# Kernel tuning notes

Hardware: AMD Instinct MI355X
Metric: run time of the kernel (lower is better)

## Reference

```python
import jax, jax.numpy as jnp
import numpy as np

T, B, Y, X, C = 9, 2, 128, 128, 64
W = (T - 1) // 2
WIN, HEADS = 8, 4
EPS = 1e-3  # keras LayerNormalization default epsilon


def _get_indices(center, size):
    right = list(range(center, size, 2))
    left = list(range(center - 2, -1, -2))
    idx = np.array(left[::-1] + right, dtype=np.int32)
    return np.clip(idx, 1, size - 2)


def _pyramid_indices(t):
    levels = []
    size, center = t, (t - 1) // 2
    while size > 1:
        c = _get_indices(center, size)
        levels.append((c - 1, c, c + 1))
        center = int(np.where(c == center)[0][0])
        size = len(c)
    return levels


LEVELS = _pyramid_indices(T)            # 3 levels for T=9: sizes 5, 3, 1
CIN = [C * (l + 1) for l in range(len(LEVELS))]    # 64, 128, 192
COUT = [C * (l + 2) for l in range(len(LEVELS))]   # 128, 192, 256


def _window_attention(q, kv, wqkv, bqkv, wo, bo):
    # WindowSpatialAttention: non-overlapping WINxWIN windows, MHA of q over kv.
    N, Yd, Xd, Cd = q.shape
    w, h = WIN, HEADS
    dh = Cd // h
    nY, nX = Yd // w, Xd // w

    def to_win(t):
        t = t.reshape(N, nY, w, nX, w, Cd).transpose(0, 1, 3, 2, 4, 5)
        return t.reshape(N * nY * nX, w * w, Cd)

    qw, kvw = to_win(q), to_win(kv)
    qp = (qw @ wqkv[0] + bqkv[0]).reshape(-1, w * w, h, dh)
    kp = (kvw @ wqkv[1] + bqkv[1]).reshape(-1, w * w, h, dh)
    vp = (kvw @ wqkv[2] + bqkv[2]).reshape(-1, w * w, h, dh)
    logits = jnp.einsum('nqhd,nkhd->nhqk', qp, kp) / jnp.sqrt(jnp.float32(dh))
    attn = jax.nn.softmax(logits, axis=-1)
    out = jnp.einsum('nhqk,nkhd->nqhd', attn, vp).reshape(-1, w * w, Cd)
    out = out @ wo + bo
    out = out.reshape(N, nY, nX, w, w, Cd).transpose(0, 1, 3, 2, 4, 5)
    return out.reshape(N, Yd, Xd, Cd)


def _forward(x, params):
    fidx = np.arange(T) - W  # relative frame indices, static (non frame-aware)
    current = x
    level1 = None
    for l, (pi, ci, ni) in enumerate(LEVELS):
        emb, lng, lnb, wqkv, bqkv, wo, bo, cw, cb = params[l]
        cin = current.shape[-1]
        # additive relative temporal embedding, indexed by frame offset + W
        t_emb = emb[fidx + W]                       # [Tl, cin]
        cur = current + t_emb[:, None, None, None, :]
        mu = cur.mean(-1, keepdims=True)
        var = cur.var(-1, keepdims=True)
        cur = (cur - mu) * jax.lax.rsqrt(var + EPS) * lng + lnb
        S = len(ci)
        prev = cur[pi].reshape(S * B, Y, X, cin)
        cen = cur[ci].reshape(S * B, Y, X, cin)
        nxt = cur[ni].reshape(S * B, Y, X, cin)
        q = jnp.concatenate([cen, prev, cen, nxt], axis=0)
        kv = jnp.concatenate([prev, cen, nxt, cen], axis=0)
        att = _window_attention(q, kv, wqkv, bqkv, wo, bo)
        parts = jnp.split(att, 4, axis=0)           # SplitBatch(n_splits=4)
        comb = jnp.concatenate(parts, axis=-1)      # Combine: concat + 1x1 conv
        down = jax.nn.relu(comb @ cw + cb)
        if S > 1:
            down = down.reshape(S, B, Y, X, down.shape[-1])
        if l == 0:
            level1 = down
        current = down
        fidx = fidx[ci]
    return current, level1


def setup_inputs() -> dict:
    key = jax.random.key(0)
    ks = iter(jax.random.split(key, 64))
    inp = {'x': jax.random.normal(next(ks), (T, B, Y, X, C), jnp.float32)}
    for l, (ci, co) in enumerate(zip(CIN, COUT)):
        inp[f'emb{l}'] = 0.02 * jax.random.normal(next(ks), (T, ci), jnp.float32)
        inp[f'lng{l}'] = jnp.ones((ci,), jnp.float32)
        inp[f'lnb{l}'] = jnp.zeros((ci,), jnp.float32)
        inp[f'wqkv{l}'] = 0.02 * jax.random.normal(next(ks), (3, ci, ci), jnp.float32)
        inp[f'bqkv{l}'] = jnp.zeros((3, ci), jnp.float32)
        inp[f'wo{l}'] = 0.02 * jax.random.normal(next(ks), (ci, ci), jnp.float32)
        inp[f'bo{l}'] = jnp.zeros((ci,), jnp.float32)
        inp[f'cw{l}'] = 0.02 * jax.random.normal(next(ks), (4 * ci, co), jnp.float32)
        inp[f'cb{l}'] = jnp.zeros((co,), jnp.float32)
    return inp


def reference(x, emb0, lng0, lnb0, wqkv0, bqkv0, wo0, bo0, cw0, cb0,
              emb1, lng1, lnb1, wqkv1, bqkv1, wo1, bo1, cw1, cb1,
              emb2, lng2, lnb2, wqkv2, bqkv2, wo2, bo2, cw2, cb2):
    params = [
        (emb0, lng0, lnb0, wqkv0, bqkv0, wo0, bo0, cw0, cb0),
        (emb1, lng1, lnb1, wqkv1, bqkv1, wo1, bo1, cw1, cb1),
        (emb2, lng2, lnb2, wqkv2, bqkv2, wo2, bo2, cw2, cb2),
    ]
    return _forward(x, params)
```

## Files before the change

kernel.cpp:

```cpp
#include <hip/hip_runtime.h>

typedef _Float16 f16;
typedef f16 f16x4 __attribute__((ext_vector_type(4)));
typedef f16 f16x8 __attribute__((ext_vector_type(8)));
typedef float f32x4 __attribute__((ext_vector_type(4)));

#define MFMA16(a, b, c) __builtin_amdgcn_mfma_f32_16x16x16f16((a), (b), (c), 0, 0, 0)
#define MFMA32(a, b, c) __builtin_amdgcn_mfma_f32_16x16x32_f16((a), (b), (c), 0, 0, 0)

struct Meta   { int pi[5], ci[5], ni[5]; };
struct EmbMap { int m[9]; };

template <int CIN>
__global__ __launch_bounds__(64) void wT_kernel(const float* __restrict__ wqkv,
                                                f16* __restrict__ wqkvT) {
  int j = blockIdx.x;
  int which = j / CIN, jj = j % CIN;
  const float* src = wqkv + (long)which * CIN * CIN + jj;
  f16* dst = wqkvT + (long)j * CIN;
  for (int c = threadIdx.x; c < CIN; c += 64) dst[c] = (f16)src[(long)c * CIN];
}

template <int CIN, int CO>
__global__ __launch_bounds__(256) void woc_kernel(
    const float* __restrict__ wo, const float* __restrict__ bo,
    const float* __restrict__ cw, const float* __restrict__ cb,
    f16* __restrict__ wocA, float* __restrict__ fb) {
  __shared__ float scw[4 * CIN];
  __shared__ float red[256];
  int o = blockIdx.x;
  for (int i = threadIdx.x; i < 4 * CIN; i += 256) scw[i] = cw[(long)i * CO + o];
  __syncthreads();
  for (int pm = threadIdx.x; pm < 4 * CIN; pm += 256) {
    int p = pm / CIN, mm = pm % CIN;
    const float* wr = wo + (long)mm * CIN;
    const float* sc = scw + p * CIN;
    float s = 0.f;
    for (int c = 0; c < CIN; ++c) s += wr[c] * sc[c];
    wocA[((long)(pm >> 3) * CO + o) * 8 + (pm & 7)] = (f16)s;
  }
  float part = 0.f;
  for (int i = threadIdx.x; i < 4 * CIN; i += 256) part += bo[i % CIN] * scw[i];
  red[threadIdx.x] = part;
  __syncthreads();
  for (int st = 128; st > 0; st >>= 1) {
    if (threadIdx.x < st) red[threadIdx.x] += red[threadIdx.x + st];
    __syncthreads();
  }
  if (threadIdx.x == 0) fb[o] = cb[o] + red[0];
}

template <typename InT, int CIN>
__global__ __launch_bounds__(256) void lnproj_kernel(
    const InT* __restrict__ in, const float* __restrict__ emb,
    const float* __restrict__ lng, const float* __restrict__ lnb,
    const f16* __restrict__ wT, const float* __restrict__ bqkv,
    f16* __restrict__ gq, f16* __restrict__ gk, f16* __restrict__ gvt,
    EmbMap em) {
  constexpr int KS = CIN / 32;
  constexpr int NT = CIN / 16;
  constexpr int C8 = CIN / 8;
  __shared__ f16 sB[CIN * CIN];
  int which = blockIdx.x;
  long win = blockIdx.y;
  long img = win >> 8;
  int wid = (int)(win & 255);
  int wy = wid >> 4, wx = wid & 15;
  int w = threadIdx.x >> 6, lane = threadIdx.x & 63;
  int r16 = lane & 15, kq = lane >> 4;
  int tok = w * 16 + r16;
  long orig = img * 16384 + (long)(wy * 8 + (tok >> 3)) * 128 + wx * 8 + (tok & 7);
  const InT* arow = in + orig * CIN + kq * 8;
  int t = (int)(img >> 1);
  const float* er = emb + (long)em.m[t] * CIN + kq * 8;

  float v[KS][8];
  float s = 0.f;
#pragma unroll
  for (int ks = 0; ks < KS; ++ks) {
    f32x4 e0 = *(const f32x4*)(er + ks * 32);
    f32x4 e1 = *(const f32x4*)(er + ks * 32 + 4);
    if constexpr (sizeof(InT) == 4) {
      f32x4 x0 = *(const f32x4*)((const float*)arow + ks * 32);
      f32x4 x1 = *(const f32x4*)((const float*)arow + ks * 32 + 4);
#pragma unroll
      for (int j = 0; j < 4; ++j) { v[ks][j] = x0[j] + e0[j]; v[ks][4 + j] = x1[j] + e1[j]; }
    } else {
      f16x8 x = *(const f16x8*)((const f16*)arow + ks * 32);
#pragma unroll
      for (int j = 0; j < 4; ++j) { v[ks][j] = (float)x[j] + e0[j]; v[ks][4 + j] = (float)x[4 + j] + e1[j]; }
    }
#pragma unroll
    for (int j = 0; j < 8; ++j) s += v[ks][j];
  }
  s += __shfl_xor(s, 16);
  s += __shfl_xor(s, 32);
  float mu = s * (1.f / CIN);
  float ssd = 0.f;
#pragma unroll
  for (int ks = 0; ks < KS; ++ks)
#pragma unroll
    for (int j = 0; j < 8; ++j) { float d = v[ks][j] - mu; ssd += d * d; }
  ssd += __shfl_xor(ssd, 16);
  ssd += __shfl_xor(ssd, 32);
  float inv = rsqrtf(ssd * (1.f / CIN) + 1e-3f);
  f16x8 a[KS];
#pragma unroll
  for (int ks = 0; ks < KS; ++ks) {
    f32x4 g0 = *(const f32x4*)(lng + ks * 32 + kq * 8);
    f32x4 g1 = *(const f32x4*)(lng + ks * 32 + kq * 8 + 4);
    f32x4 b0 = *(const f32x4*)(lnb + ks * 32 + kq * 8);
    f32x4 b1 = *(const f32x4*)(lnb + ks * 32 + kq * 8 + 4);
#pragma unroll
    for (int j = 0; j < 4; ++j) {
      a[ks][j] = (f16)((v[ks][j] - mu) * inv * g0[j] + b0[j]);
      a[ks][4 + j] = (f16)((v[ks][4 + j] - mu) * inv * g1[j] + b1[j]);
    }
  }

  const f16* wsrc = wT + (long)which * CIN * CIN;
  for (int idx = threadIdx.x; idx < CIN * C8; idx += 256) {
    int j = idx / C8, c8 = idx % C8;
    f16x8 vv = *(const f16x8*)(wsrc + idx * 8);
    int off = ((j * CIN + c8 * 8) * 2) ^ ((j & 7) << 4);
    *(f16x8*)((char*)sB + off) = vv;
  }
  __syncthreads();

  f32x4 acc[NT] = {};
#pragma unroll
  for (int ks = 0; ks < KS; ++ks) {
#pragma unroll
    for (int tt = 0; tt < NT; ++tt) {
      int off = (((tt * 16 + r16) * CIN + ks * 32 + kq * 8) * 2) ^ ((r16 & 7) << 4);
      f16x8 bb = *(const f16x8*)((char*)sB + off);
      acc[tt] = MFMA32(a[ks], bb, acc[tt]);
    }
  }
  __syncthreads();

  if (which < 2) {
#pragma unroll
    for (int tt = 0; tt < NT; ++tt) {
      float bias = bqkv[which * CIN + tt * 16 + r16];
#pragma unroll
      for (int rg = 0; rg < 4; ++rg) {
        int r = w * 16 + kq * 4 + rg;
        int c = tt * 16 + r16;
        int off = ((r * CIN + c) * 2) ^ ((r & 7) << 4);
        *(f16*)((char*)sB + off) = (f16)(acc[tt][rg] + bias);
      }
    }
    __syncthreads();
    f16* dst = (which ? gk : gq) + win * 64 * CIN;
    for (int idx = threadIdx.x; idx < 64 * C8; idx += 256) {
      int r = idx / C8, c8 = idx % C8;
      int off = ((r * CIN + c8 * 8) * 2) ^ ((r & 7) << 4);
      f16x8 vv = *(const f16x8*)((char*)sB + off);
      *(f16x8*)(dst + r * CIN + c8 * 8) = vv;
    }
  } else {
#pragma unroll
    for (int tt = 0; tt < NT; ++tt) {
      float bias = bqkv[2 * CIN + tt * 16 + r16];
#pragma unroll
      for (int rg = 0; rg < 4; ++rg) {
        int c = tt * 16 + r16;
        int pos = w * 16 + kq * 4 + rg;
        int off = ((c * 64 + pos) * 2) ^ ((c & 7) << 4);
        *(f16*)((char*)sB + off) = (f16)(acc[tt][rg] + bias);
      }
    }
    __syncthreads();
    for (int c = threadIdx.x; c < CIN; c += 256) {
      f16* dst = gvt + (win * CIN + c) * 64;
#pragma unroll
      for (int p8 = 0; p8 < 8; ++p8) {
        int off = ((c * 64 + p8 * 8) * 2) ^ ((c & 7) << 4);
        *(f16x8*)(dst + p8 * 8) = *(const f16x8*)((char*)sB + off);
      }
    }
  }
}

template <int CIN, int DH, int CO>
__global__ __launch_bounds__(256) void attn4_kernel(
    const f16* __restrict__ gq, const f16* __restrict__ gk,
    const f16* __restrict__ gvt, const f16* __restrict__ wocA,
    const float* __restrict__ fb, float* __restrict__ out, Meta m) {
  constexpr int NKS = DH / 16;
  constexpr int NK8 = DH / 32;
  constexpr int NK4 = (DH % 32) / 16;
  constexpr int CO4 = CO / 4;
  constexpr int NTC = CO4 / 16;
  constexpr int NKD = 4 * CIN / 32;
  constexpr float scale = (DH == 16) ? 0.25f : (DH == 32) ? 0.1767766952966369f
                                                          : 0.1443375672974064f;
  constexpr float escale = scale * 1.4426950408889634f;
  __shared__ f16 O[4][64 * CIN];

  int img = blockIdx.y;
  int sidx = img >> 1, b = img & 1;
  int wid = blockIdx.x;
  int wy = wid >> 4, wx = wid & 15;
  int p = threadIdx.x >> 6, lane = threadIdx.x & 63;
  int r16 = lane & 15, kq = lane >> 4;
  int fpi = m.pi[sidx], fci = m.ci[sidx], fni = m.ni[sidx];

  int qfr = (p == 1) ? fpi : ((p == 3) ? fni : fci);
  int kfr = (p == 0) ? fpi : ((p == 2) ? fni : fci);
  long qwin = (long)((qfr * 2 + b) * 256 + wid);
  long kwin = (long)((kfr * 2 + b) * 256 + wid);
  char* Ob = (char*)O[p];

#pragma unroll
  for (int hh = 0; hh < 4; ++hh) {
    f16x8 kf8[4][NK8 ? NK8 : 1];
    f16x4 kf4[4][NK4 ? NK4 : 1];
#pragma unroll
    for (int tj = 0; tj < 4; ++tj) {
      const f16* kb = gk + (kwin * 64 + tj * 16 + r16) * CIN + hh * DH;
      if constexpr (NK8 > 0)
#pragma unroll
        for (int n = 0; n < NK8; ++n)
          kf8[tj][n] = *(const f16x8*)(kb + n * 32 + kq * 8);
      if constexpr (NK4 > 0)
#pragma unroll
        for (int n = 0; n < NK4; ++n)
          kf4[tj][n] = *(const f16x4*)(kb + NK8 * 32 + n * 16 + kq * 4);
    }
    f16x4 va[NKS][4];
#pragma unroll
    for (int dt = 0; dt < NKS; ++dt)
#pragma unroll
      for (int jt = 0; jt < 4; ++jt)
        va[dt][jt] = *(const f16x4*)(gvt + (kwin * CIN + hh * DH + dt * 16 + r16) * 64 +
                                     jt * 16 + kq * 4);

    f16x4 pa[4][4];
#pragma unroll
    for (int ti = 0; ti < 4; ++ti) {
      const f16* qb = gq + (qwin * 64 + ti * 16 + r16) * CIN + hh * DH;
      f32x4 s4[4] = {};
      if constexpr (NK8 > 0) {
        f16x8 qf8[NK8];
#pragma unroll
        for (int n = 0; n < NK8; ++n) qf8[n] = *(const f16x8*)(qb + n * 32 + kq * 8);
#pragma unroll
        for (int tj = 0; tj < 4; ++tj)
#pragma unroll
          for (int n = 0; n < NK8; ++n) s4[tj] = MFMA32(kf8[tj][n], qf8[n], s4[tj]);
      }
      if constexpr (NK4 > 0) {
        f16x4 qf4[NK4];
#pragma unroll
        for (int n = 0; n < NK4; ++n)
          qf4[n] = *(const f16x4*)(qb + NK8 * 32 + n * 16 + kq * 4);
#pragma unroll
        for (int tj = 0; tj < 4; ++tj)
#pragma unroll
          for (int n = 0; n < NK4; ++n) s4[tj] = MFMA16(kf4[tj][n], qf4[n], s4[tj]);
      }
      float sum = 0.f;
#pragma unroll
      for (int tj = 0; tj < 4; ++tj)
#pragma unroll
        for (int rg = 0; rg < 4; ++rg) {
          float e = __builtin_amdgcn_exp2f(s4[tj][rg] * escale);
          s4[tj][rg] = e;
          sum += e;
        }
      sum += __shfl_xor(sum, 16);
      sum += __shfl_xor(sum, 32);
      float invs = 1.f / sum;
#pragma unroll
      for (int tj = 0; tj < 4; ++tj) {
        f16x4 pv;
#pragma unroll
        for (int rg = 0; rg < 4; ++rg) pv[rg] = (f16)(s4[tj][rg] * invs);
        pa[tj][ti] = pv;
      }
    }

#pragma unroll
    for (int dt = 0; dt < NKS; ++dt) {
#pragma unroll
      for (int ti = 0; ti < 4; ++ti) {
        f32x4 po = {};
#pragma unroll
        for (int jt = 0; jt < 4; ++jt) po = MFMA16(va[dt][jt], pa[jt][ti], po);
        int i = ti * 16 + r16;
        int c0 = hh * DH + dt * 16 + kq * 4;
        f16x4 pk;
#pragma unroll
        for (int rg = 0; rg < 4; ++rg) pk[rg] = (f16)po[rg];
        int off = ((i * CIN + c0) * 2) ^ ((i & 7) << 4);
        *(f16x4*)(Ob + off) = pk;
      }
    }
  }
  __syncthreads();

  f32x4 dn[NTC][4] = {};
#pragma unroll
  for (int ck = 0; ck < NKD; ++ck) {
    int k0 = ck * 32;
    int psrc = k0 / CIN;
    int c = k0 - psrc * CIN;
    char* Osrc = (char*)O[psrc];
    f16x8 ob[4];
#pragma unroll
    for (int ti = 0; ti < 4; ++ti) {
      int i = ti * 16 + r16;
      int off = ((i * CIN + c + kq * 8) * 2) ^ ((i & 7) << 4);
      ob[ti] = *(const f16x8*)(Osrc + off);
    }
    long pm = (long)(k0 + kq * 8);
#pragma unroll
    for (int ot = 0; ot < NTC; ++ot) {
      f16x8 wa = *(const f16x8*)(wocA + ((pm >> 3) * CO + p * CO4 + ot * 16 + r16) * 8);
#pragma unroll
      for (int ti = 0; ti < 4; ++ti) dn[ot][ti] = MFMA32(wa, ob[ti], dn[ot][ti]);
    }
  }

#pragma unroll
  for (int ot = 0; ot < NTC; ++ot) {
    f32x4 fb4 = *(const f32x4*)(fb + p * CO4 + ot * 16 + kq * 4);
#pragma unroll
    for (int ti = 0; ti < 4; ++ti) {
      int i = ti * 16 + r16;
      long gtok = (long)img * 16384 + (wy * 8 + (i >> 3)) * 128 + wx * 8 + (i & 7);
      f32x4 vv;
#pragma unroll
      for (int rg = 0; rg < 4; ++rg) vv[rg] = fmaxf(dn[ot][ti][rg] + fb4[rg], 0.f);
      *(f32x4*)(out + gtok * CO + p * CO4 + ot * 16 + kq * 4) = vv;
    }
  }
}

template <int CIN, int DH, int CO>
__global__ __launch_bounds__(256) void attn_kernel(
    const f16* __restrict__ gq, const f16* __restrict__ gk,
    const f16* __restrict__ gvt, const f16* __restrict__ wocA,
    const float* __restrict__ fb, float* __restrict__ out, Meta m) {
  constexpr int NKS = DH / 16;
  constexpr int NK8 = DH / 32;
  constexpr int NK4 = (DH % 32) / 16;
  constexpr int CO4 = CO / 4;
  constexpr int NTC = CO4 / 16;
  constexpr int NKD = CIN / 32;
  constexpr float scale = (DH == 16) ? 0.25f : (DH == 32) ? 0.1767766952966369f
                                                          : 0.1443375672974064f;
  constexpr float escale = scale * 1.4426950408889634f;
  __shared__ f16 O[2][64 * CIN];

  int img = blockIdx.y;
  int sidx = img >> 1, b = img & 1;
  int wid = blockIdx.x;
  int wy = wid >> 4, wx = wid & 15;
  int h = threadIdx.x >> 6, lane = threadIdx.x & 63;
  int r16 = lane & 15, kq = lane >> 4;
  int fpi = m.pi[sidx], fci = m.ci[sidx], fni = m.ni[sidx];

  f32x4 dn[NTC][4] = {};

#pragma unroll
  for (int p = 0; p < 4; ++p) {
    int qfr = (p == 1) ? fpi : ((p == 3) ? fni : fci);
    int kfr = (p == 0) ? fpi : ((p == 2) ? fni : fci);
    long qwin = (long)((qfr * 2 + b) * 256 + wid);
    long kwin = (long)((kfr * 2 + b) * 256 + wid);

    f16x8 kf8[4][NK8 ? NK8 : 1];
    f16x4 kf4[4][NK4 ? NK4 : 1];
#pragma unroll
    for (int tj = 0; tj < 4; ++tj) {
      const f16* kb = gk + (kwin * 64 + tj * 16 + r16) * CIN + h * DH;
      if constexpr (NK8 > 0)
#pragma unroll
        for (int n = 0; n < NK8; ++n)
          kf8[tj][n] = *(const f16x8*)(kb + n * 32 + kq * 8);
      if constexpr (NK4 > 0)
#pragma unroll
        for (int n = 0; n < NK4; ++n)
          kf4[tj][n] = *(const f16x4*)(kb + NK8 * 32 + n * 16 + kq * 4);
    }
    f16x4 va[NKS][4];
#pragma unroll
    for (int dt = 0; dt < NKS; ++dt)
#pragma unroll
      for (int jt = 0; jt < 4; ++jt)
        va[dt][jt] = *(const f16x4*)(gvt + (kwin * CIN + h * DH + dt * 16 + r16) * 64 +
                                     jt * 16 + kq * 4);

    f16x4 pa[4][4];
#pragma unroll
    for (int ti = 0; ti < 4; ++ti) {
      const f16* qb = gq + (qwin * 64 + ti * 16 + r16) * CIN + h * DH;
      f32x4 s4[4] = {};
      if constexpr (NK8 > 0) {
        f16x8 qf8[NK8];
#pragma unroll
        for (int n = 0; n < NK8; ++n) qf8[n] = *(const f16x8*)(qb + n * 32 + kq * 8);
#pragma unroll
        for (int tj = 0; tj < 4; ++tj)
#pragma unroll
          for (int n = 0; n < NK8; ++n) s4[tj] = MFMA32(kf8[tj][n], qf8[n], s4[tj]);
      }
      if constexpr (NK4 > 0) {
        f16x4 qf4[NK4];
#pragma unroll
        for (int n = 0; n < NK4; ++n)
          qf4[n] = *(const f16x4*)(qb + NK8 * 32 + n * 16 + kq * 4);
#pragma unroll
        for (int tj = 0; tj < 4; ++tj)
#pragma unroll
          for (int n = 0; n < NK4; ++n) s4[tj] = MFMA16(kf4[tj][n], qf4[n], s4[tj]);
      }
      float sum = 0.f;
#pragma unroll
      for (int tj = 0; tj < 4; ++tj)
#pragma unroll
        for (int rg = 0; rg < 4; ++rg) {
          float e = __builtin_amdgcn_exp2f(s4[tj][rg] * escale);
          s4[tj][rg] = e;
          sum += e;
        }
      sum += __shfl_xor(sum, 16);
      sum += __shfl_xor(sum, 32);
      float invs = 1.f / sum;
#pragma unroll
      for (int tj = 0; tj < 4; ++tj) {
        f16x4 pv;
#pragma unroll
        for (int rg = 0; rg < 4; ++rg) pv[rg] = (f16)(s4[tj][rg] * invs);
        pa[tj][ti] = pv;
      }
    }

    char* Ob = (char*)O[p & 1];
#pragma unroll
    for (int dt = 0; dt < NKS; ++dt) {
#pragma unroll
      for (int ti = 0; ti < 4; ++ti) {
        f32x4 po = {};
#pragma unroll
        for (int jt = 0; jt < 4; ++jt) po = MFMA16(va[dt][jt], pa[jt][ti], po);
        int i = ti * 16 + r16;
        int c0 = h * DH + dt * 16 + kq * 4;
        f16x4 pk;
#pragma unroll
        for (int rg = 0; rg < 4; ++rg) pk[rg] = (f16)po[rg];
        int off = ((i * CIN + c0) * 2) ^ ((i & 7) << 4);
        *(f16x4*)(Ob + off) = pk;
      }
    }
    __syncthreads();

#pragma unroll
    for (int ck = 0; ck < NKD; ++ck) {
      f16x8 ob[4];
#pragma unroll
      for (int ti = 0; ti < 4; ++ti) {
        int i = ti * 16 + r16;
        int off = ((i * CIN + ck * 32 + kq * 8) * 2) ^ ((i & 7) << 4);
        ob[ti] = *(const f16x8*)(Ob + off);
      }
      long pm = (long)(p * CIN + ck * 32 + kq * 8);
#pragma unroll
      for (int ot = 0; ot < NTC; ++ot) {
        f16x8 wa = *(const f16x8*)(wocA + ((pm >> 3) * CO + h * CO4 + ot * 16 + r16) * 8);
#pragma unroll
        for (int ti = 0; ti < 4; ++ti) dn[ot][ti] = MFMA32(wa, ob[ti], dn[ot][ti]);
      }
    }
  }

#pragma unroll
  for (int ot = 0; ot < NTC; ++ot) {
    f32x4 fb4 = *(const f32x4*)(fb + h * CO4 + ot * 16 + kq * 4);
#pragma unroll
    for (int ti = 0; ti < 4; ++ti) {
      int i = ti * 16 + r16;
      long gtok = (long)img * 16384 + (wy * 8 + (i >> 3)) * 128 + wx * 8 + (i & 7);
      f32x4 vv;
#pragma unroll
      for (int rg = 0; rg < 4; ++rg) vv[rg] = fmaxf(dn[ot][ti][rg] + fb4[rg], 0.f);
      *(f32x4*)(out + gtok * CO + h * CO4 + ot * 16 + kq * 4) = vv;
    }
  }
}

extern "C" void kernel_launch(void* const* d_in, const int* in_sizes, int n_in,
                              void* d_out, int out_size, void* d_ws, size_t ws_size,
                              hipStream_t stream) {
  const float* x = (const float*)d_in[0];
#define PRM(l, k) ((const float*)d_in[1 + 9 * (l) + (k)])
  float* outCur = (float*)d_out;
  float* outL1 = (float*)d_out + 8388608;

  char* ws = (char*)d_ws;
  const size_t OFF_B = 125829120ull;
  const size_t OFF_W = OFF_B + 75497472ull;
  f16* qkvbase = (f16*)ws;
  float* accum1 = (float*)(ws + OFF_B);
  f16* wqkvT = (f16*)(ws + OFF_W);
  f16* wocA = (f16*)(ws + OFF_W + 262144);
  float* fb = (float*)(ws + OFF_W + 262144 + 524288);

  Meta m0 = {{0, 1, 3, 5, 6}, {1, 2, 4, 6, 7}, {2, 3, 5, 7, 8}};
  Meta m1 = {{0, 1, 2, 0, 0}, {1, 2, 3, 0, 0}, {2, 3, 4, 0, 0}};
  Meta m2 = {{0, 0, 0, 0, 0}, {1, 0, 0, 0, 0}, {2, 0, 0, 0, 0}};
  EmbMap em0 = {{0, 1, 2, 3, 4, 5, 6, 7, 8}};
  EmbMap em1 = {{1, 2, 4, 6, 7, 0, 0, 0, 0}};
  EmbMap em2 = {{2, 4, 6, 0, 0, 0, 0, 0, 0}};

  {
    constexpr int CIN = 64, DH = 16, CO = 128, TL = 9, S = 5;
    long ntok = (long)TL * 2 * 16384;
    f16 *gq = qkvbase, *gk = gq + ntok * CIN, *gvt = gk + ntok * CIN;
    wT_kernel<CIN><<<dim3(3 * CIN), 64, 0, stream>>>(PRM(0, 3), wqkvT);
    woc_kernel<CIN, CO><<<dim3(CO), 256, 0, stream>>>(PRM(0, 5), PRM(0, 6), PRM(0, 7), PRM(0, 8), wocA, fb);
    lnproj_kernel<float, CIN><<<dim3(3, (unsigned)(ntok / 64)), 256, 0, stream>>>(
        x, PRM(0, 0), PRM(0, 1), PRM(0, 2), wqkvT, PRM(0, 4), gq, gk, gvt, em0);
    attn4_kernel<CIN, DH, CO><<<dim3(256, S * 2), 256, 0, stream>>>(
        gq, gk, gvt, wocA, fb, outL1, m0);
  }
  {
    constexpr int CIN = 128, DH = 32, CO = 192, TL = 5, S = 3;
    long ntok = (long)TL * 2 * 16384;
    f16 *gq = qkvbase, *gk = gq + ntok * CIN, *gvt = gk + ntok * CIN;
    wT_kernel<CIN><<<dim3(3 * CIN), 64, 0, stream>>>(PRM(1, 3), wqkvT);
    woc_kernel<CIN, CO><<<dim3(CO), 256, 0, stream>>>(PRM(1, 5), PRM(1, 6), PRM(1, 7), PRM(1, 8), wocA, fb);
    lnproj_kernel<float, CIN><<<dim3(3, (unsigned)(ntok / 64)), 256, 0, stream>>>(
        outL1, PRM(1, 0), PRM(1, 1), PRM(1, 2), wqkvT, PRM(1, 4), gq, gk, gvt, em1);
    attn4_kernel<CIN, DH, CO><<<dim3(256, S * 2), 256, 0, stream>>>(
        gq, gk, gvt, wocA, fb, accum1, m1);
  }
  {
    constexpr int CIN = 192, DH = 48, CO = 256, TL = 3, S = 1;
    long ntok = (long)TL * 2 * 16384;
    f16 *gq = qkvbase, *gk = gq + ntok * CIN, *gvt = gk + ntok * CIN;
    wT_kernel<CIN><<<dim3(3 * CIN), 64, 0, stream>>>(PRM(2, 3), wqkvT);
    woc_kernel<CIN, CO><<<dim3(CO), 256, 0, stream>>>(PRM(2, 5), PRM(2, 6), PRM(2, 7), PRM(2, 8), wocA, fb);
    lnproj_kernel<float, CIN><<<dim3(3, (unsigned)(ntok / 64)), 256, 0, stream>>>(
        accum1, PRM(2, 0), PRM(2, 1), PRM(2, 2), wqkvT, PRM(2, 4), gq, gk, gvt, em2);
    attn_kernel<CIN, DH, CO><<<dim3(256, S * 2), 256, 0, stream>>>(
        gq, gk, gvt, wocA, fb, outCur, m2);
  }
#undef PRM
}
```

Before: 662.3 us.

## Halve attn4 shared memory via two-phase pair processing; split lnproj output columns

The attention kernel used to keep all four frame-pair outputs in shared memory at once. It now processes two pairs per phase, with each warp taking two heads, and runs the output-projection MFMAs once per phase so only half the shared buffer is needed. The aim is to cut LDS use and raise occupancy, at the cost of an extra barrier. Separately, the level-2 LN+projection kernel (CIN=192) now splits its output columns across two blocks, so each block holds only half the weight tile in shared memory. This recomputes LayerNorm in both blocks and adds a padded-stride layout for the non-power-of-two slice width.

```diff
diff --git a/kernel.cpp b/kernel.cpp
--- a/kernel.cpp
+++ b/kernel.cpp
@@ -50,7 +50,7 @@
   if (threadIdx.x == 0) fb[o] = cb[o] + red[0];
 }
 
-template <typename InT, int CIN>
+template <typename InT, int CIN, int NSPLIT>
 __global__ __launch_bounds__(256) void lnproj_kernel(
     const InT* __restrict__ in, const float* __restrict__ emb,
     const float* __restrict__ lng, const float* __restrict__ lnb,
@@ -58,10 +58,14 @@
     f16* __restrict__ gq, f16* __restrict__ gk, f16* __restrict__ gvt,
     EmbMap em) {
   constexpr int KS = CIN / 32;
-  constexpr int NT = CIN / 16;
+  constexpr int SL = CIN / NSPLIT;
+  constexpr int NTS = SL / 16;
   constexpr int C8 = CIN / 8;
-  __shared__ f16 sB[CIN * CIN];
-  int which = blockIdx.x;
+  constexpr int SL8 = SL / 8;
+  constexpr int SLP = (SL & (SL - 1)) ? 128 : SL;
+  __shared__ f16 sB[SL * CIN];
+  int which = blockIdx.x / NSPLIT;
+  int half = blockIdx.x % NSPLIT;
   long win = blockIdx.y;
   long img = win >> 8;
   int wid = (int)(win & 255);
@@ -118,8 +122,8 @@
     }
   }
 
-  const f16* wsrc = wT + (long)which * CIN * CIN;
-  for (int idx = threadIdx.x; idx < CIN * C8; idx += 256) {
+  const f16* wsrc = wT + ((long)which * CIN + half * SL) * CIN;
+  for (int idx = threadIdx.x; idx < SL * C8; idx += 256) {
     int j = idx / C8, c8 = idx % C8;
     f16x8 vv = *(const f16x8*)(wsrc + idx * 8);
     int off = ((j * CIN + c8 * 8) * 2) ^ ((j & 7) << 4);
@@ -127,12 +131,13 @@
   }
   __syncthreads();
 
-  f32x4 acc[NT] = {};
+  f32x4 acc[NTS] = {};
 #pragma unroll
   for (int ks = 0; ks < KS; ++ks) {
 #pragma unroll
-    for (int tt = 0; tt < NT; ++tt) {
-      int off = (((tt * 16 + r16) * CIN + ks * 32 + kq * 8) * 2) ^ ((r16 & 7) << 4);
+    for (int tt = 0; tt < NTS; ++tt) {
+      int jl = tt * 16 + r16;
+      int off = ((jl * CIN + ks * 32 + kq * 8) * 2) ^ ((jl & 7) << 4);
       f16x8 bb = *(const f16x8*)((char*)sB + off);
       acc[tt] = MFMA32(a[ks], bb, acc[tt]);
     }
@@ -141,28 +146,28 @@
 
   if (which < 2) {
 #pragma unroll
-    for (int tt = 0; tt < NT; ++tt) {
-      float bias = bqkv[which * CIN + tt * 16 + r16];
+    for (int tt = 0; tt < NTS; ++tt) {
+      float bias = bqkv[which * CIN + half * SL + tt * 16 + r16];
 #pragma unroll
       for (int rg = 0; rg < 4; ++rg) {
         int r = w * 16 + kq * 4 + rg;
         int c = tt * 16 + r16;
-        int off = ((r * CIN + c) * 2) ^ ((r & 7) << 4);
+        int off = ((r * SLP + c) * 2) ^ ((r & 7) << 4);
         *(f16*)((char*)sB + off) = (f16)(acc[tt][rg] + bias);
       }
     }
     __syncthreads();
-    f16* dst = (which ? gk : gq) + win * 64 * CIN;
-    for (int idx = threadIdx.x; idx < 64 * C8; idx += 256) {
-      int r = idx / C8, c8 = idx % C8;
-      int off = ((r * CIN + c8 * 8) * 2) ^ ((r & 7) << 4);
+    f16* dst = (which ? gk : gq) + win * 64 * CIN + half * SL;
+    for (int idx = threadIdx.x; idx < 64 * SL8; idx += 256) {
+      int r = idx / SL8, c8 = idx % SL8;
+      int off = ((r * SLP + c8 * 8) * 2) ^ ((r & 7) << 4);
       f16x8 vv = *(const f16x8*)((char*)sB + off);
       *(f16x8*)(dst + r * CIN + c8 * 8) = vv;
     }
   } else {
 #pragma unroll
-    for (int tt = 0; tt < NT; ++tt) {
-      float bias = bqkv[2 * CIN + tt * 16 + r16];
+    for (int tt = 0; tt < NTS; ++tt) {
+      float bias = bqkv[2 * CIN + half * SL + tt * 16 + r16];
 #pragma unroll
       for (int rg = 0; rg < 4; ++rg) {
         int c = tt * 16 + r16;
@@ -172,8 +177,8 @@
       }
     }
     __syncthreads();
-    for (int c = threadIdx.x; c < CIN; c += 256) {
-      f16* dst = gvt + (win * CIN + c) * 64;
+    for (int c = threadIdx.x; c < SL; c += 256) {
+      f16* dst = gvt + (win * CIN + half * SL + c) * 64;
 #pragma unroll
       for (int p8 = 0; p8 < 8; ++p8) {
         int off = ((c * 64 + p8 * 8) * 2) ^ ((c & 7) << 4);
@@ -193,140 +198,147 @@
   constexpr int NK4 = (DH % 32) / 16;
   constexpr int CO4 = CO / 4;
   constexpr int NTC = CO4 / 16;
-  constexpr int NKD = 4 * CIN / 32;
+  constexpr int NKD = 2 * CIN / 32;
   constexpr float scale = (DH == 16) ? 0.25f : (DH == 32) ? 0.1767766952966369f
                                                           : 0.1443375672974064f;
   constexpr float escale = scale * 1.4426950408889634f;
-  __shared__ f16 O[4][64 * CIN];
+  __shared__ f16 O[2][64 * CIN];
 
   int img = blockIdx.y;
   int sidx = img >> 1, b = img & 1;
   int wid = blockIdx.x;
   int wy = wid >> 4, wx = wid & 15;
-  int p = threadIdx.x >> 6, lane = threadIdx.x & 63;
+  int w = threadIdx.x >> 6, lane = threadIdx.x & 63;
   int r16 = lane & 15, kq = lane >> 4;
   int fpi = m.pi[sidx], fci = m.ci[sidx], fni = m.ni[sidx];
-
-  int qfr = (p == 1) ? fpi : ((p == 3) ? fni : fci);
-  int kfr = (p == 0) ? fpi : ((p == 2) ? fni : fci);
-  long qwin = (long)((qfr * 2 + b) * 256 + wid);
-  long kwin = (long)((kfr * 2 + b) * 256 + wid);
-  char* Ob = (char*)O[p];
-
-#pragma unroll
-  for (int hh = 0; hh < 4; ++hh) {
-    f16x8 kf8[4][NK8 ? NK8 : 1];
-    f16x4 kf4[4][NK4 ? NK4 : 1];
-#pragma unroll
-    for (int tj = 0; tj < 4; ++tj) {
-      const f16* kb = gk + (kwin * 64 + tj * 16 + r16) * CIN + hh * DH;
-      if constexpr (NK8 > 0)
-#pragma unroll
-        for (int n = 0; n < NK8; ++n)
-          kf8[tj][n] = *(const f16x8*)(kb + n * 32 + kq * 8);
-      if constexpr (NK4 > 0)
-#pragma unroll
-        for (int n = 0; n < NK4; ++n)
-          kf4[tj][n] = *(const f16x4*)(kb + NK8 * 32 + n * 16 + kq * 4);
-    }
-    f16x4 va[NKS][4];
-#pragma unroll
-    for (int dt = 0; dt < NKS; ++dt)
-#pragma unroll
-      for (int jt = 0; jt < 4; ++jt)
-        va[dt][jt] = *(const f16x4*)(gvt + (kwin * CIN + hh * DH + dt * 16 + r16) * 64 +
-                                     jt * 16 + kq * 4);
-
-    f16x4 pa[4][4];
-#pragma unroll
-    for (int ti = 0; ti < 4; ++ti) {
-      const f16* qb = gq + (qwin * 64 + ti * 16 + r16) * CIN + hh * DH;
-      f32x4 s4[4] = {};
-      if constexpr (NK8 > 0) {
-        f16x8 qf8[NK8];
-#pragma unroll
-        for (int n = 0; n < NK8; ++n) qf8[n] = *(const f16x8*)(qb + n * 32 + kq * 8);
+  char* Ob = (char*)O[w >> 1];
+
+  f32x4 dn[NTC][4] = {};
+
+#pragma unroll
+  for (int ph = 0; ph < 2; ++ph) {
+    int p = ph * 2 + (w >> 1);
+    int qfr = (p == 1) ? fpi : ((p == 3) ? fni : fci);
+    int kfr = (p == 0) ? fpi : ((p == 2) ? fni : fci);
+    long qwin = (long)((qfr * 2 + b) * 256 + wid);
+    long kwin = (long)((kfr * 2 + b) * 256 + wid);
+
+#pragma unroll
+    for (int hi = 0; hi < 2; ++hi) {
+      int hh = (w & 1) * 2 + hi;
+      f16x8 kf8[4][NK8 ? NK8 : 1];
+      f16x4 kf4[4][NK4 ? NK4 : 1];
+#pragma unroll
+      for (int tj = 0; tj < 4; ++tj) {
+        const f16* kb = gk + (kwin * 64 + tj * 16 + r16) * CIN + hh * DH;
+        if constexpr (NK8 > 0)
+#pragma unroll
+          for (int n = 0; n < NK8; ++n)
+            kf8[tj][n] = *(const f16x8*)(kb + n * 32 + kq * 8);
+        if constexpr (NK4 > 0)
+#pragma unroll
+          for (int n = 0; n < NK4; ++n)
+            kf4[tj][n] = *(const f16x4*)(kb + NK8 * 32 + n * 16 + kq * 4);
+      }
+      f16x4 va[NKS][4];
+#pragma unroll
+      for (int dt = 0; dt < NKS; ++dt)
+#pragma unroll
+        for (int jt = 0; jt < 4; ++jt)
+          va[dt][jt] = *(const f16x4*)(gvt + (kwin * CIN + hh * DH + dt * 16 + r16) * 64 +
+                                       jt * 16 + kq * 4);
+
+      f16x4 pa[4][4];
+#pragma unroll
+      for (int ti = 0; ti < 4; ++ti) {
+        const f16* qb = gq + (qwin * 64 + ti * 16 + r16) * CIN + hh * DH;
+        f32x4 s4[4] = {};
+        if constexpr (NK8 > 0) {
+          f16x8 qf8[NK8];
+#pragma unroll
+          for (int n = 0; n < NK8; ++n) qf8[n] = *(const f16x8*)(qb + n * 32 + kq * 8);
+#pragma unroll
+          for (int tj = 0; tj < 4; ++tj)
+#pragma unroll
+            for (int n = 0; n < NK8; ++n) s4[tj] = MFMA32(kf8[tj][n], qf8[n], s4[tj]);
+        }
+        if constexpr (NK4 > 0) {
+          f16x4 qf4[NK4];
+#pragma unroll
+          for (int n = 0; n < NK4; ++n)
+            qf4[n] = *(const f16x4*)(qb + NK8 * 32 + n * 16 + kq * 4);
+#pragma unroll
+          for (int tj = 0; tj < 4; ++tj)
+#pragma unroll
+            for (int n = 0; n < NK4; ++n) s4[tj] = MFMA16(kf4[tj][n], qf4[n], s4[tj]);
+        }
+        float sum = 0.f;
 #pragma unroll
         for (int tj = 0; tj < 4; ++tj)
 #pragma unroll
-          for (int n = 0; n < NK8; ++n) s4[tj] = MFMA32(kf8[tj][n], qf8[n], s4[tj]);
-      }
-      if constexpr (NK4 > 0) {
-        f16x4 qf4[NK4];
-#pragma unroll
-        for (int n = 0; n < NK4; ++n)
-          qf4[n] = *(const f16x4*)(qb + NK8 * 32 + n * 16 + kq * 4);
-#pragma unroll
-        for (int tj = 0; tj < 4; ++tj)
-#pragma unroll
-          for (int n = 0; n < NK4; ++n) s4[tj] = MFMA16(kf4[tj][n], qf4[n], s4[tj]);
-      }
-      float sum = 0.f;
-#pragma unroll
-      for (int tj = 0; tj < 4; ++tj)
-#pragma unroll
-        for (int rg = 0; rg < 4; ++rg) {
-          float e = __builtin_amdgcn_exp2f(s4[tj][rg] * escale);
-          s4[tj][rg] = e;
-          sum += e;
+          for (int rg = 0; rg < 4; ++rg) {
+            float e = __builtin_amdgcn_exp2f(s4[tj][rg] * escale);
+            s4[tj][rg] = e;
+            sum += e;
+          }
+        sum += __shfl_xor(sum, 16);
+        sum += __shfl_xor(sum, 32);
+        float invs = 1.f / sum;
+#pragma unroll
+        for (int tj = 0; tj < 4; ++tj) {
+          f16x4 pv;
+#pragma unroll
+          for (int rg = 0; rg < 4; ++rg) pv[rg] = (f16)(s4[tj][rg] * invs);
+          pa[tj][ti] = pv;
         }
-      sum += __shfl_xor(sum, 16);
-      sum += __shfl_xor(sum, 32);
-      float invs = 1.f / sum;
-#pragma unroll
-      for (int tj = 0; tj < 4; ++tj) {
-        f16x4 pv;
-#pragma unroll
-        for (int rg = 0; rg < 4; ++rg) pv[rg] = (f16)(s4[tj][rg] * invs);
-        pa[tj][ti] = pv;
-      }
-    }
-
-#pragma unroll
-    for (int dt = 0; dt < NKS; ++dt) {
+      }
+
+#pragma unroll
+      for (int dt = 0; dt < NKS; ++dt) {
+#pragma unroll
+        for (int ti = 0; ti < 4; ++ti) {
+          f32x4 po = {};
+#pragma unroll
+          for (int jt = 0; jt < 4; ++jt) po = MFMA16(va[dt][jt], pa[jt][ti], po);
+          int i = ti * 16 + r16;
+          int c0 = hh * DH + dt * 16 + kq * 4;
+          f16x4 pk;
+#pragma unroll
+          for (int rg = 0; rg < 4; ++rg) pk[rg] = (f16)po[rg];
+          int off = ((i * CIN + c0) * 2) ^ ((i & 7) << 4);
+          *(f16x4*)(Ob + off) = pk;
+        }
+      }
+    }
+    __syncthreads();
+
+#pragma unroll
+    for (int ck = 0; ck < NKD; ++ck) {
+      int k0 = ck * 32;
+      int pl = k0 / CIN;
+      int c = k0 - pl * CIN;
+      char* Osrc = (char*)O[pl];
+      f16x8 ob[4];
 #pragma unroll
       for (int ti = 0; ti < 4; ++ti) {
-        f32x4 po = {};
-#pragma unroll
-        for (int jt = 0; jt < 4; ++jt) po = MFMA16(va[dt][jt], pa[jt][ti], po);
         int i = ti * 16 + r16;
-        int c0 = hh * DH + dt * 16 + kq * 4;
-        f16x4 pk;
-#pragma unroll
-        for (int rg = 0; rg < 4; ++rg) pk[rg] = (f16)po[rg];
-        int off = ((i * CIN + c0) * 2) ^ ((i & 7) << 4);
-        *(f16x4*)(Ob + off) = pk;
-      }
-    }
-  }
-  __syncthreads();
-
-  f32x4 dn[NTC][4] = {};
-#pragma unroll
-  for (int ck = 0; ck < NKD; ++ck) {
-    int k0 = ck * 32;
-    int psrc = k0 / CIN;
-    int c = k0 - psrc * CIN;
-    char* Osrc = (char*)O[psrc];
-    f16x8 ob[4];
-#pragma unroll
-    for (int ti = 0; ti < 4; ++ti) {
-      int i = ti * 16 + r16;
-      int off = ((i * CIN + c + kq * 8) * 2) ^ ((i & 7) << 4);
-      ob[ti] = *(const f16x8*)(Osrc + off);
-    }
-    long pm = (long)(k0 + kq * 8);
-#pragma unroll
-    for (int ot = 0; ot < NTC; ++ot) {
-      f16x8 wa = *(const f16x8*)(wocA + ((pm >> 3) * CO + p * CO4 + ot * 16 + r16) * 8);
-#pragma unroll
-      for (int ti = 0; ti < 4; ++ti) dn[ot][ti] = MFMA32(wa, ob[ti], dn[ot][ti]);
-    }
+        int off = ((i * CIN + c + kq * 8) * 2) ^ ((i & 7) << 4);
+        ob[ti] = *(const f16x8*)(Osrc + off);
+      }
+      long pm = (long)((ph * 2 + pl) * CIN + c + kq * 8);
+#pragma unroll
+      for (int ot = 0; ot < NTC; ++ot) {
+        f16x8 wa = *(const f16x8*)(wocA + ((pm >> 3) * CO + w * CO4 + ot * 16 + r16) * 8);
+#pragma unroll
+        for (int ti = 0; ti < 4; ++ti) dn[ot][ti] = MFMA32(wa, ob[ti], dn[ot][ti]);
+      }
+    }
+    if (ph == 0) __syncthreads();
   }
 
 #pragma unroll
   for (int ot = 0; ot < NTC; ++ot) {
-    f32x4 fb4 = *(const f32x4*)(fb + p * CO4 + ot * 16 + kq * 4);
+    f32x4 fb4 = *(const f32x4*)(fb + w * CO4 + ot * 16 + kq * 4);
 #pragma unroll
     for (int ti = 0; ti < 4; ++ti) {
       int i = ti * 16 + r16;
@@ -334,7 +346,7 @@
       f32x4 vv;
 #pragma unroll
       for (int rg = 0; rg < 4; ++rg) vv[rg] = fmaxf(dn[ot][ti][rg] + fb4[rg], 0.f);
-      *(f32x4*)(out + gtok * CO + p * CO4 + ot * 16 + kq * 4) = vv;
+      *(f32x4*)(out + gtok * CO + w * CO4 + ot * 16 + kq * 4) = vv;
     }
   }
 }
@@ -522,7 +534,7 @@
     f16 *gq = qkvbase, *gk = gq + ntok * CIN, *gvt = gk + ntok * CIN;
     wT_kernel<CIN><<<dim3(3 * CIN), 64, 0, stream>>>(PRM(0, 3), wqkvT);
     woc_kernel<CIN, CO><<<dim3(CO), 256, 0, stream>>>(PRM(0, 5), PRM(0, 6), PRM(0, 7), PRM(0, 8), wocA, fb);
-    lnproj_kernel<float, CIN><<<dim3(3, (unsigned)(ntok / 64)), 256, 0, stream>>>(
+    lnproj_kernel<float, CIN, 1><<<dim3(3, (unsigned)(ntok / 64)), 256, 0, stream>>>(
         x, PRM(0, 0), PRM(0, 1), PRM(0, 2), wqkvT, PRM(0, 4), gq, gk, gvt, em0);
     attn4_kernel<CIN, DH, CO><<<dim3(256, S * 2), 256, 0, stream>>>(
         gq, gk, gvt, wocA, fb, outL1, m0);
@@ -533,7 +545,7 @@
     f16 *gq = qkvbase, *gk = gq + ntok * CIN, *gvt = gk + ntok * CIN;
     wT_kernel<CIN><<<dim3(3 * CIN), 64, 0, stream>>>(PRM(1, 3), wqkvT);
     woc_kernel<CIN, CO><<<dim3(CO), 256, 0, stream>>>(PRM(1, 5), PRM(1, 6), PRM(1, 7), PRM(1, 8), wocA, fb);
-    lnproj_kernel<float, CIN><<<dim3(3, (unsigned)(ntok / 64)), 256, 0, stream>>>(
+    lnproj_kernel<float, CIN, 1><<<dim3(3, (unsigned)(ntok / 64)), 256, 0, stream>>>(
         outL1, PRM(1, 0), PRM(1, 1), PRM(1, 2), wqkvT, PRM(1, 4), gq, gk, gvt, em1);
     attn4_kernel<CIN, DH, CO><<<dim3(256, S * 2), 256, 0, stream>>>(
         gq, gk, gvt, wocA, fb, accum1, m1);
@@ -544,7 +556,7 @@
     f16 *gq = qkvbase, *gk = gq + ntok * CIN, *gvt = gk + ntok * CIN;
     wT_kernel<CIN><<<dim3(3 * CIN), 64, 0, stream>>>(PRM(2, 3), wqkvT);
     woc_kernel<CIN, CO><<<dim3(CO), 256, 0, stream>>>(PRM(2, 5), PRM(2, 6), PRM(2, 7), PRM(2, 8), wocA, fb);
-    lnproj_kernel<float, CIN><<<dim3(3, (unsigned)(ntok / 64)), 256, 0, stream>>>(
+    lnproj_kernel<float, CIN, 2><<<dim3(6, (unsigned)(ntok / 64)), 256, 0, stream>>>(
         accum1, PRM(2, 0), PRM(2, 1), PRM(2, 2), wqkvT, PRM(2, 4), gq, gk, gvt, em2);
     attn_kernel<CIN, DH, CO><<<dim3(256, S * 2), 256, 0, stream>>>(
         gq, gk, gvt, wocA, fb, outCur, m2);
```

New measurement: 683.8 us. 1.03x slower.
